# Performance work log

Measured on AMD Instinct MI355X. Metric: run time of the kernel, lower is better.

The kernel has to match this reference:

```python
import jax, jax.numpy as jnp
import numpy as np

NUM_HEADS = 16
HIDDEN = 1024
HEAD_DIM = HIDDEN // NUM_HEADS


def setup_inputs() -> dict:
    key = jax.random.key(0)
    ks = jax.random.split(key, 9)
    B, S, D = 2, 2048, HIDDEN
    scale = 1.0 / np.sqrt(D)
    inp = {
        "X": jax.random.normal(ks[0], (B, S, D), dtype=jnp.float32),
        "Wq": jax.random.normal(ks[1], (D, D), dtype=jnp.float32) * scale,
        "bq": jnp.zeros((D,), dtype=jnp.float32),
        "Wk": jax.random.normal(ks[2], (D, D), dtype=jnp.float32) * scale,
        "bk": jnp.zeros((D,), dtype=jnp.float32),
        "Wv": jax.random.normal(ks[3], (D, D), dtype=jnp.float32) * scale,
        "bv": jnp.zeros((D,), dtype=jnp.float32),
        "Wo": jax.random.normal(ks[4], (D, D), dtype=jnp.float32) * scale,
        "bo": jnp.zeros((D,), dtype=jnp.float32),
    }
    return inp


def _split_heads(x):
    b, s, d = x.shape
    return x.reshape(b, s, NUM_HEADS, HEAD_DIM).transpose(0, 2, 1, 3)  # [b,h,s,hd]


def reference(X, Wq, bq, Wk, bk, Wv, bv, Wo, bo):
    b, s, d = X.shape
    q = _split_heads(X @ Wq + bq)
    k = _split_heads(X @ Wk + bk)
    v = _split_heads(X @ Wv + bv)
    scores = jnp.einsum("bhqd,bhkd->bhqk", q, k) / jnp.sqrt(jnp.float32(HEAD_DIM))
    causal = jnp.tril(jnp.ones((s, s), dtype=bool))
    scores = jnp.where(causal[None, None], scores, jnp.float32(-jnp.inf))
    attn = jax.nn.softmax(scores, axis=-1)
    out = jnp.einsum("bhqk,bhkd->bhqd", attn, v)
    out = out.transpose(0, 2, 1, 3).reshape(b, s, d)
    return out @ Wo + bo
```

## Files before the change

kernel.cpp:

```cpp
#include <hip/hip_runtime.h>
#include <hip/hip_bf16.h>

#define S_LEN 2048
#define D_MODEL 1024
#define NHEAD 16
#define HDIM 64
#define BATCH 2
#define M_TOT (BATCH * S_LEN)
#define KVB 64

typedef __attribute__((ext_vector_type(4))) float f32x4;
typedef __attribute__((ext_vector_type(4))) short s16x4;
typedef __attribute__((ext_vector_type(8))) short s16x8;

#define AS1 __attribute__((address_space(1)))
#define AS3 __attribute__((address_space(3)))

#define SC2 0.18033688011112042f

__device__ inline short f2bf(float f) {
  unsigned u = __float_as_uint(f);
  return (short)((u + 0x7fffu + ((u >> 16) & 1u)) >> 16);
}

__device__ __forceinline__ unsigned cvtpk(float lo, float hi) {
  unsigned r;
  asm("v_cvt_pk_bf16_f32 %0, %1, %2" : "=v"(r) : "v"(lo), "v"(hi));
  return r;
}
__device__ __forceinline__ s16x4 pk4(float a, float b, float c, float d) {
  union { unsigned u[2]; s16x4 s; } x;
  x.u[0] = cvtpk(a, b);
  x.u[1] = cvtpk(c, d);
  return x.s;
}

__device__ __forceinline__ void gl_lds16(const short* g, short* l) {
  __builtin_amdgcn_global_load_lds((const AS1 void*)g, (AS3 void*)l, 16, 0, 0);
}

__global__ __launch_bounds__(256) void xcast_k(const float* __restrict__ X,
                                               short* __restrict__ Xb) {
  const size_t i = ((size_t)blockIdx.x * 256 + threadIdx.x) * 8;
  float4 a = *(const float4*)&X[i];
  float4 b = *(const float4*)&X[i + 4];
  s16x8 p;
  p[0] = f2bf(a.x); p[1] = f2bf(a.y); p[2] = f2bf(a.z); p[3] = f2bf(a.w);
  p[4] = f2bf(b.x); p[5] = f2bf(b.y); p[6] = f2bf(b.z); p[7] = f2bf(b.w);
  *(s16x8*)&Xb[i] = p;
}

__global__ __launch_bounds__(256) void wtrans_k(const float* __restrict__ W0,
                                                const float* __restrict__ W1,
                                                const float* __restrict__ W2,
                                                const float* __restrict__ W3,
                                                short* __restrict__ Wcat) {
  const int z = blockIdx.z;
  const float* W = z == 0 ? W0 : z == 1 ? W1 : z == 2 ? W2 : W3;
  short* Wt = Wcat + (size_t)z * D_MODEL * D_MODEL;
  const float scl = (z == 0) ? SC2 : 1.f;
  __shared__ float tile[32][33];
  const int tx = threadIdx.x, ty = threadIdx.y;
  const int n0 = blockIdx.x * 32, k0 = blockIdx.y * 32;
#pragma unroll
  for (int j = 0; j < 4; ++j)
    tile[ty + j * 8][tx] = W[(size_t)(k0 + ty + j * 8) * D_MODEL + n0 + tx];
  __syncthreads();
#pragma unroll
  for (int j = 0; j < 4; ++j)
    Wt[(size_t)(n0 + ty + j * 8) * D_MODEL + k0 + tx] =
        f2bf(tile[tx][ty + j * 8] * scl);
}

__global__ __launch_bounds__(256, 2) void gemm_qkv_k(
    const short* __restrict__ Xb, const short* __restrict__ Wcat,
    const float* __restrict__ bq, const float* __restrict__ bk,
    const float* __restrict__ bv, short* __restrict__ Qb,
    short* __restrict__ Kb, short* __restrict__ Vtb) {
  __shared__ short As[2 * 128 * 64];
  __shared__ short Bs[2 * 192 * 64];
  const int orig = blockIdx.x;
  const int xcd = orig & 7;
  const int k = orig >> 3;
  const int m0 = (((xcd & 3) << 3) + (k & 7)) * 128;
  const int n0 = (((xcd >> 2) << 3) + (k >> 3)) * 192;

  const int tid = threadIdx.x;
  const int lane = tid & 63, w = tid >> 6;
  const int wm = w >> 1, wn = w & 1;
  const int lr = lane & 15, lg = lane >> 4;
  const int lr8 = lane >> 3;
  const int sl = lane & 7;
  const int scol = ((sl ^ lr8) << 3);

  f32x4 acc[4][6] = {};

  auto stage = [&](int buf, int k0) {
#pragma unroll
    for (int j = 0; j < 4; ++j) {
      const int rb = j * 4 + w;
      const int row = rb * 8 + lr8;
      gl_lds16(&Xb[(size_t)(m0 + row) * D_MODEL + k0 + scol],
               &As[buf * 8192 + rb * 512]);
    }
#pragma unroll
    for (int j = 0; j < 6; ++j) {
      const int rb = j * 4 + w;
      const int row = rb * 8 + lr8;
      gl_lds16(&Wcat[(size_t)(n0 + row) * D_MODEL + k0 + scol],
               &Bs[buf * 12288 + rb * 512]);
    }
  };

  stage(0, 0);
  __syncthreads();

  for (int t = 0; t < D_MODEL / 64; ++t) {
    const int cur = t & 1;
    if (t + 1 < D_MODEL / 64) stage(cur ^ 1, (t + 1) * 64);
    const short* Ac = As + cur * 8192;
    const short* Bc = Bs + cur * 12288;
#pragma unroll
    for (int ks = 0; ks < 2; ++ks) {
      s16x8 af[4], bfr[6];
#pragma unroll
      for (int i = 0; i < 4; ++i) {
        const int Ra = wm * 64 + i * 16 + lr;
        af[i] = *(const s16x8*)&Ac[Ra * 64 + ((((ks << 2) | lg) ^ (Ra & 7)) << 3)];
      }
#pragma unroll
      for (int i = 0; i < 6; ++i) {
        const int Rb = wn * 96 + i * 16 + lr;
        bfr[i] = *(const s16x8*)&Bc[Rb * 64 + ((((ks << 2) | lg) ^ (Rb & 7)) << 3)];
      }
      __builtin_amdgcn_s_setprio(1);
#pragma unroll
      for (int mi = 0; mi < 4; ++mi)
#pragma unroll
        for (int ni = 0; ni < 6; ++ni)
          acc[mi][ni] = __builtin_amdgcn_mfma_f32_16x16x32_bf16(
              af[mi], bfr[ni], acc[mi][ni], 0, 0, 0);
      __builtin_amdgcn_s_setprio(0);
    }
    __syncthreads();
  }

#pragma unroll
  for (int ni = 0; ni < 6; ++ni) {
    const int n = n0 + wn * 96 + ni * 16 + lr;
    const int z = n >> 10;
    const float bn = (z == 0 ? bq[n & 1023] * SC2
                             : (z == 1 ? bk[n & 1023] : bv[n & 1023]));
    short* Cp = z == 0 ? Qb : z == 1 ? Kb : Vtb;
    const int h = (n >> 6) & 15, d = n & 63;
#pragma unroll
    for (int mi = 0; mi < 4; ++mi) {
      const int mb = m0 + wm * 64 + mi * 16 + lg * 4;
      f32x4 v = acc[mi][ni];
      if (z < 2) {
#pragma unroll
        for (int j = 0; j < 4; ++j) {
          int m = mb + j;
          int b = m >> 11, s = m & 2047;
          Cp[((size_t)((b * NHEAD + h) * S_LEN) + s) * HDIM + d] = f2bf(v[j] + bn);
        }
      } else {
        int b = mb >> 11, s = mb & 2047;
        s16x4 p;
#pragma unroll
        for (int j = 0; j < 4; ++j) p[j] = f2bf(v[j] + bn);
        *(s16x4*)&Cp[((size_t)((b * NHEAD + h) * HDIM) + d) * S_LEN + s] = p;
      }
    }
  }
}

__global__ __launch_bounds__(256, 2) void gemm_o_k(const short* __restrict__ A,
                                                   const short* __restrict__ Bt,
                                                   const float* __restrict__ bias,
                                                   float* __restrict__ C) {
  __shared__ short As[2 * 128 * 64];
  __shared__ short Bs[2 * 64 * 64];
  const int orig = blockIdx.x;
  const int xcd = orig & 7;
  const int k = orig >> 3;
  const int m0 = (((xcd & 3) << 3) + (k & 7)) * 128;
  const int n0 = (((xcd >> 2) << 3) + (k >> 3)) * 64;

  const int tid = threadIdx.x;
  const int lane = tid & 63, w = tid >> 6;
  const int wm = w >> 1, wn = w & 1;
  const int lr = lane & 15, lg = lane >> 4;
  const int lr8 = lane >> 3;
  const int sl = lane & 7;
  const int scol = ((sl ^ lr8) << 3);

  f32x4 acc[4][2] = {};

  auto stage = [&](int buf, int k0) {
#pragma unroll
    for (int j = 0; j < 4; ++j) {
      const int rb = j * 4 + w;
      const int row = rb * 8 + lr8;
      gl_lds16(&A[(size_t)(m0 + row) * D_MODEL + k0 + scol],
               &As[buf * 8192 + rb * 512]);
    }
#pragma unroll
    for (int j = 0; j < 2; ++j) {
      const int rb = j * 4 + w;
      const int row = rb * 8 + lr8;
      gl_lds16(&Bt[(size_t)(n0 + row) * D_MODEL + k0 + scol],
               &Bs[buf * 4096 + rb * 512]);
    }
  };

  stage(0, 0);
  __syncthreads();

  for (int t = 0; t < D_MODEL / 64; ++t) {
    const int cur = t & 1;
    if (t + 1 < D_MODEL / 64) stage(cur ^ 1, (t + 1) * 64);
    const short* Ac = As + cur * 8192;
    const short* Bc = Bs + cur * 4096;
#pragma unroll
    for (int ks = 0; ks < 2; ++ks) {
      s16x8 af[4], bfr[2];
#pragma unroll
      for (int i = 0; i < 4; ++i) {
        const int Ra = wm * 64 + i * 16 + lr;
        af[i] = *(const s16x8*)&Ac[Ra * 64 + ((((ks << 2) | lg) ^ (Ra & 7)) << 3)];
      }
#pragma unroll
      for (int i = 0; i < 2; ++i) {
        const int Rb = wn * 32 + i * 16 + lr;
        bfr[i] = *(const s16x8*)&Bc[Rb * 64 + ((((ks << 2) | lg) ^ (Rb & 7)) << 3)];
      }
      __builtin_amdgcn_s_setprio(1);
#pragma unroll
      for (int mi = 0; mi < 4; ++mi)
#pragma unroll
        for (int ni = 0; ni < 2; ++ni)
          acc[mi][ni] = __builtin_amdgcn_mfma_f32_16x16x32_bf16(
              af[mi], bfr[ni], acc[mi][ni], 0, 0, 0);
      __builtin_amdgcn_s_setprio(0);
    }
    __syncthreads();
  }

#pragma unroll
  for (int ni = 0; ni < 2; ++ni) {
    const int n = n0 + wn * 32 + ni * 16 + lr;
    const float bn = bias[n];
#pragma unroll
    for (int mi = 0; mi < 4; ++mi) {
      const int mb = m0 + wm * 64 + mi * 16 + lg * 4;
      f32x4 v = acc[mi][ni];
#pragma unroll
      for (int j = 0; j < 4; ++j)
        C[(size_t)(mb + j) * D_MODEL + n] = v[j] + bn;
    }
  }
}

__global__ __launch_bounds__(256, 4) void attn_k(const short* __restrict__ Q,
                                                 const short* __restrict__ K,
                                                 const short* __restrict__ Vt,
                                                 short* __restrict__ AO) {
  __shared__ short Ks[2][KVB * HDIM];
  __shared__ short Vs[2][HDIM * KVB];
  const int tid = threadIdx.x, w = tid >> 6, lane = tid & 63;
  const int lr = lane & 15, lg = lane >> 4;
  const int orig = blockIdx.x;
  const int wg = (orig & 7) * 128 + (orig >> 3);
  const int bh = wg >> 5, qi = wg & 31;
  const int qt = (bh & 1) ? qi : 31 - qi;
  const int q0 = qt * 64, nt = qt + 1;
  const int b = bh >> 4, h = bh & 15;
  const size_t headQK = (size_t)bh * S_LEN * HDIM;
  const size_t headV = (size_t)bh * HDIM * S_LEN;
  const int qrow = q0 + w * 16 + lr;

  const int l8 = lane >> 3, sl = lane & 7;
  const int scol = ((sl ^ l8) << 3);

  auto stage = [&](int kv0, int buf) {
#pragma unroll
    for (int j = 0; j < 2; ++j) {
      const int rb = w * 2 + j;
      const int row = rb * 8 + l8;
      gl_lds16(&K[headQK + (size_t)(kv0 + row) * HDIM + scol],
               &Ks[buf][rb * 512]);
      gl_lds16(&Vt[headV + (size_t)row * S_LEN + kv0 + scol],
               &Vs[buf][rb * 512]);
    }
  };

  const s16x8 qf0 = *(const s16x8*)&Q[headQK + (size_t)qrow * HDIM + lg * 8];
  const s16x8 qf1 = *(const s16x8*)&Q[headQK + (size_t)qrow * HDIM + 32 + lg * 8];

  f32x4 o[4] = {};
  float m_run = -1e30f;
  float l_part = 0.f;

  stage(0, 0);
  __syncthreads();

  for (int t = 0; t < nt; ++t) {
    if (t + 1 < nt) stage((t + 1) * KVB, (t + 1) & 1);
    const short* Kc = Ks[t & 1];
    const short* Vc = Vs[t & 1];
    const bool diag = (t == nt - 1);
    const int gmax = diag ? (w + 1) : 4;

    f32x4 sc[4];
    __builtin_amdgcn_s_setprio(1);
#pragma unroll
    for (int g = 0; g < 4; ++g) {
      if (g < gmax) {
        const int R = g * 16 + lr;
        const s16x8 kf0 = *(const s16x8*)&Kc[R * 64 + ((lg ^ (lr & 7)) << 3)];
        const s16x8 kf1 = *(const s16x8*)&Kc[R * 64 + (((4 | lg) ^ (lr & 7)) << 3)];
        f32x4 z = {0.f, 0.f, 0.f, 0.f};
        sc[g] = __builtin_amdgcn_mfma_f32_16x16x32_bf16(kf0, qf0, z, 0, 0, 0);
        sc[g] = __builtin_amdgcn_mfma_f32_16x16x32_bf16(kf1, qf1, sc[g], 0, 0, 0);
      }
    }
    __builtin_amdgcn_s_setprio(0);

    if (diag) {
#pragma unroll
      for (int g = 0; g < 4; ++g)
        if (g == w) {
#pragma unroll
          for (int j = 0; j < 4; ++j)
            if (lg * 4 + j > lr) sc[g][j] = -1e30f;
        }
    }

    float tm = -1e30f;
#pragma unroll
    for (int g = 0; g < 4; ++g)
      if (g < gmax)
        tm = fmaxf(tm, fmaxf(fmaxf(sc[g][0], sc[g][1]),
                             fmaxf(sc[g][2], sc[g][3])));

    if (!__all(tm <= m_run + 8.f)) {
      float tr = fmaxf(tm, m_run);
      tr = fmaxf(tr, __shfl_xor(tr, 16));
      tr = fmaxf(tr, __shfl_xor(tr, 32));
      const float corr = __builtin_amdgcn_exp2f(m_run - tr);
      l_part *= corr;
#pragma unroll
      for (int dc = 0; dc < 4; ++dc) o[dc] = o[dc] * corr;
      m_run = tr;
    }

    s16x4 pf[4];
#pragma unroll
    for (int g = 0; g < 4; ++g) {
      if (g < gmax) {
        const float e0 = __builtin_amdgcn_exp2f(sc[g][0] - m_run);
        const float e1 = __builtin_amdgcn_exp2f(sc[g][1] - m_run);
        const float e2 = __builtin_amdgcn_exp2f(sc[g][2] - m_run);
        const float e3 = __builtin_amdgcn_exp2f(sc[g][3] - m_run);
        pf[g] = pk4(e0, e1, e2, e3);
        l_part += (e0 + e1) + (e2 + e3);
      }
    }

    __builtin_amdgcn_s_setprio(1);
#pragma unroll
    for (int g = 0; g < 4; ++g) {
      if (g < gmax) {
#pragma unroll
        for (int dc = 0; dc < 4; ++dc) {
          const int row = dc * 16 + lr;
          const s16x4 vf = *(const s16x4*)&Vc[row * 64 +
              (((2 * g + (lg >> 1)) ^ (lr & 7)) << 3) + ((lg & 1) << 2)];
          o[dc] = __builtin_amdgcn_mfma_f32_16x16x16bf16_1k(vf, pf[g], o[dc], 0, 0, 0);
        }
      }
    }
    __builtin_amdgcn_s_setprio(0);
    __syncthreads();
  }

  float lt = l_part;
  lt += __shfl_xor(lt, 16);
  lt += __shfl_xor(lt, 32);
  const float inv = 1.f / lt;
#pragma unroll
  for (int dc = 0; dc < 4; ++dc) {
    s16x4 pk;
#pragma unroll
    for (int j = 0; j < 4; ++j) pk[j] = f2bf(o[dc][j] * inv);
    *(s16x4*)&AO[((size_t)(b * S_LEN + qrow)) * D_MODEL + h * HDIM + dc * 16 + lg * 4] = pk;
  }
}

extern "C" void kernel_launch(void* const* d_in, const int* in_sizes, int n_in,
                              void* d_out, int out_size, void* d_ws, size_t ws_size,
                              hipStream_t stream) {
  const float* X  = (const float*)d_in[0];
  const float* Wq = (const float*)d_in[1];
  const float* bq = (const float*)d_in[2];
  const float* Wk = (const float*)d_in[3];
  const float* bk = (const float*)d_in[4];
  const float* Wv = (const float*)d_in[5];
  const float* bv = (const float*)d_in[6];
  const float* Wo = (const float*)d_in[7];
  const float* bo = (const float*)d_in[8];
  (void)in_sizes; (void)n_in; (void)out_size; (void)ws_size;

  char* ws = (char*)d_ws;
  const size_t WSZ = (size_t)D_MODEL * D_MODEL * sizeof(short);
  const size_t QSZ = (size_t)M_TOT * D_MODEL * sizeof(short);
  short* Wcat = (short*)ws;
  short* Qb  = (short*)(ws + 4 * WSZ);
  short* Kb  = (short*)(ws + 4 * WSZ + QSZ);
  short* Vtb = (short*)(ws + 4 * WSZ + 2 * QSZ);
  short* AO  = (short*)(ws + 4 * WSZ + 3 * QSZ);
  short* Xb  = AO;
  short* Wto = Wcat + 3 * (size_t)D_MODEL * D_MODEL;

  xcast_k<<<dim3(M_TOT * D_MODEL / 2048), 256, 0, stream>>>(X, Xb);
  wtrans_k<<<dim3(32, 32, 4), dim3(32, 8), 0, stream>>>(Wq, Wk, Wv, Wo, Wcat);

  gemm_qkv_k<<<dim3(512), 256, 0, stream>>>(Xb, Wcat, bq, bk, bv,
                                            Qb, Kb, Vtb);

  attn_k<<<dim3(1024), 256, 0, stream>>>(Qb, Kb, Vtb, AO);

  gemm_o_k<<<dim3(512), 256, 0, stream>>>(AO, Wto, bo, (float*)d_out);
}
```

Baseline: 105.7 us.

## Prefetch two tiles ahead with explicit vmcnt waits in GEMMs and attention

The three kernels (QKV GEMM, output GEMM, attention) now issue loads for the next two tiles before entering the loop. Each iteration waits with s_waitcnt vmcnt(N) only for the older tile's direct-to-LDS loads, then uses raw s_barrier plus sched_barrier in place of __syncthreads. This gives a deeper in-flight load queue, so global-to-LDS copies overlap a full compute step instead of one. It depends on the hand-counted vmcnt values matching the exact number of loads each stage issues; a wrong count would create a race.

```diff
diff --git a/kernel.cpp b/kernel.cpp
--- a/kernel.cpp
+++ b/kernel.cpp
@@ -17,6 +17,8 @@
 #define AS3 __attribute__((address_space(3)))
 
 #define SC2 0.18033688011112042f
+
+#define WAITVM(N) asm volatile("s_waitcnt vmcnt(" #N ")" ::: "memory")
 
 __device__ inline short f2bf(float f) {
   unsigned u = __float_as_uint(f);
@@ -113,11 +115,13 @@
   };
 
   stage(0, 0);
-  __syncthreads();
+  stage(1, 64);
 
   for (int t = 0; t < D_MODEL / 64; ++t) {
     const int cur = t & 1;
-    if (t + 1 < D_MODEL / 64) stage(cur ^ 1, (t + 1) * 64);
+    if (t + 1 < D_MODEL / 64) { WAITVM(10); } else { WAITVM(0); }
+    __builtin_amdgcn_s_barrier();
+    __builtin_amdgcn_sched_barrier(0);
     const short* Ac = As + cur * 8192;
     const short* Bc = Bs + cur * 12288;
 #pragma unroll
@@ -142,7 +146,9 @@
               af[mi], bfr[ni], acc[mi][ni], 0, 0, 0);
       __builtin_amdgcn_s_setprio(0);
     }
-    __syncthreads();
+    __builtin_amdgcn_sched_barrier(0);
+    __builtin_amdgcn_s_barrier();
+    if (t + 2 < D_MODEL / 64) stage(cur, (t + 2) * 64);
   }
 
 #pragma unroll
@@ -215,11 +221,13 @@
   };
 
   stage(0, 0);
-  __syncthreads();
+  stage(1, 64);
 
   for (int t = 0; t < D_MODEL / 64; ++t) {
     const int cur = t & 1;
-    if (t + 1 < D_MODEL / 64) stage(cur ^ 1, (t + 1) * 64);
+    if (t + 1 < D_MODEL / 64) { WAITVM(6); } else { WAITVM(0); }
+    __builtin_amdgcn_s_barrier();
+    __builtin_amdgcn_sched_barrier(0);
     const short* Ac = As + cur * 8192;
     const short* Bc = Bs + cur * 4096;
 #pragma unroll
@@ -244,7 +252,9 @@
               af[mi], bfr[ni], acc[mi][ni], 0, 0, 0);
       __builtin_amdgcn_s_setprio(0);
     }
-    __syncthreads();
+    __builtin_amdgcn_sched_barrier(0);
+    __builtin_amdgcn_s_barrier();
+    if (t + 2 < D_MODEL / 64) stage(cur, (t + 2) * 64);
   }
 
 #pragma unroll
@@ -252,7 +262,7 @@
     const int n = n0 + wn * 32 + ni * 16 + lr;
     const float bn = bias[n];
 #pragma unroll
-    for (int mi = 0; mi < 4; ++mi) {
+    for (int mi = 0; mi < 2 * 2; ++mi) {
       const int mb = m0 + wm * 64 + mi * 16 + lg * 4;
       f32x4 v = acc[mi][ni];
 #pragma unroll
@@ -303,10 +313,12 @@
   float l_part = 0.f;
 
   stage(0, 0);
-  __syncthreads();
+  if (nt > 1) stage(KVB, 1);
 
   for (int t = 0; t < nt; ++t) {
-    if (t + 1 < nt) stage((t + 1) * KVB, (t + 1) & 1);
+    if (t + 1 < nt) { WAITVM(4); } else { WAITVM(0); }
+    __builtin_amdgcn_s_barrier();
+    __builtin_amdgcn_sched_barrier(0);
     const short* Kc = Ks[t & 1];
     const short* Vc = Vs[t & 1];
     const bool diag = (t == nt - 1);
@@ -382,7 +394,9 @@
       }
     }
     __builtin_amdgcn_s_setprio(0);
-    __syncthreads();
+    __builtin_amdgcn_sched_barrier(0);
+    __builtin_amdgcn_s_barrier();
+    if (t + 2 < nt) stage((t + 2) * KVB, t & 1);
   }
 
   float lt = l_part;
```

New measurement: 103.5 us. -2.1%, faster.

## Split KV range of long causal query tiles across two blocks with combine kernel

Applied to the files above, without the earlier changes.

Query tiles in the second half of the sequence now have their KV loop split into two halves, each run by a separate workgroup. The halves write unnormalized fp32 partial outputs plus running max and sum into scratch, and a new combine kernel merges them into bf16 attention output. The aim is to shorten the critical path of the longest causal tiles and balance work across CUs. The cost is an extra kernel launch, the fp32 partial traffic, and the loss of the previous heavy-first block ordering. Scratch is borrowed from the output buffer and from the already-consumed Wq region of the workspace.

```diff
diff --git a/kernel.cpp b/kernel.cpp
--- a/kernel.cpp
+++ b/kernel.cpp
@@ -265,16 +265,28 @@
 __global__ __launch_bounds__(256, 4) void attn_k(const short* __restrict__ Q,
                                                  const short* __restrict__ K,
                                                  const short* __restrict__ Vt,
-                                                 short* __restrict__ AO) {
+                                                 short* __restrict__ AO,
+                                                 float* __restrict__ opart,
+                                                 float* __restrict__ lmbuf) {
   __shared__ short Ks[2][KVB * HDIM];
   __shared__ short Vs[2][HDIM * KVB];
   const int tid = threadIdx.x, w = tid >> 6, lane = tid & 63;
   const int lr = lane & 15, lg = lane >> 4;
   const int orig = blockIdx.x;
-  const int wg = (orig & 7) * 128 + (orig >> 3);
-  const int bh = wg >> 5, qi = wg & 31;
-  const int qt = (bh & 1) ? qi : 31 - qi;
-  const int q0 = qt * 64, nt = qt + 1;
+  const int bh = orig & 31;
+  const int job = orig >> 5;
+  int qt, part, t0, te;
+  if (job < 16) {
+    qt = job; part = -1; t0 = 0; te = qt + 1;
+  } else {
+    qt = 16 + ((job - 16) >> 1);
+    part = (job - 16) & 1;
+    const int ntl = qt + 1, h0 = ntl >> 1;
+    t0 = part ? h0 : 0;
+    te = part ? ntl : h0;
+  }
+  const int nt = qt + 1;
+  const int q0 = qt * 64;
   const int b = bh >> 4, h = bh & 15;
   const size_t headQK = (size_t)bh * S_LEN * HDIM;
   const size_t headV = (size_t)bh * HDIM * S_LEN;
@@ -302,11 +314,11 @@
   float m_run = -1e30f;
   float l_part = 0.f;
 
-  stage(0, 0);
+  stage(t0 * KVB, t0 & 1);
   __syncthreads();
 
-  for (int t = 0; t < nt; ++t) {
-    if (t + 1 < nt) stage((t + 1) * KVB, (t + 1) & 1);
+  for (int t = t0; t < te; ++t) {
+    if (t + 1 < te) stage((t + 1) * KVB, (t + 1) & 1);
     const short* Kc = Ks[t & 1];
     const short* Vc = Vs[t & 1];
     const bool diag = (t == nt - 1);
@@ -388,13 +400,61 @@
   float lt = l_part;
   lt += __shfl_xor(lt, 16);
   lt += __shfl_xor(lt, 32);
-  const float inv = 1.f / lt;
-#pragma unroll
-  for (int dc = 0; dc < 4; ++dc) {
+
+  if (part < 0) {
+    const float inv = 1.f / lt;
+#pragma unroll
+    for (int dc = 0; dc < 4; ++dc) {
+      s16x4 pk;
+#pragma unroll
+      for (int j = 0; j < 4; ++j) pk[j] = f2bf(o[dc][j] * inv);
+      *(s16x4*)&AO[((size_t)(b * S_LEN + qrow)) * D_MODEL + h * HDIM + dc * 16 + lg * 4] = pk;
+    }
+  } else {
+    const int p = (bh * 16 + (qt - 16)) * 2 + part;
+    float* ob = opart + (size_t)p * 4096;
+    const int rloc = w * 16 + lr;
+#pragma unroll
+    for (int dc = 0; dc < 4; ++dc)
+      *(f32x4*)&ob[rloc * 64 + dc * 16 + lg * 4] = o[dc];
+    if (lane < 16) {
+      float* lm = lmbuf + (size_t)p * 128;
+      lm[rloc * 2 + 0] = m_run;
+      lm[rloc * 2 + 1] = lt;
+    }
+  }
+}
+
+__global__ __launch_bounds__(256) void attn_combine_k(
+    const float* __restrict__ opart, const float* __restrict__ lmbuf,
+    short* __restrict__ AO) {
+  const int blk = blockIdx.x;
+  const int bh = blk & 31, s = blk >> 5;
+  const int qt = 16 + s;
+  const int p0 = (bh * 16 + s) * 2;
+  const int tid = threadIdx.x;
+  const int r = tid >> 2, d0 = (tid & 3) * 16;
+  const float m0 = lmbuf[(size_t)p0 * 128 + r * 2];
+  const float l0 = lmbuf[(size_t)p0 * 128 + r * 2 + 1];
+  const float m1 = lmbuf[(size_t)(p0 + 1) * 128 + r * 2];
+  const float l1 = lmbuf[(size_t)(p0 + 1) * 128 + r * 2 + 1];
+  const float M = fmaxf(m0, m1);
+  const float w0 = __builtin_amdgcn_exp2f(m0 - M);
+  const float w1 = __builtin_amdgcn_exp2f(m1 - M);
+  const float inv = 1.f / (l0 * w0 + l1 * w1);
+  const float* o0 = opart + (size_t)p0 * 4096 + r * 64 + d0;
+  const float* o1 = opart + (size_t)(p0 + 1) * 4096 + r * 64 + d0;
+  const int b = bh >> 4, h = bh & 15;
+  const int qrow = qt * 64 + r;
+  short* dst = AO + ((size_t)(b * S_LEN + qrow)) * D_MODEL + h * HDIM + d0;
+#pragma unroll
+  for (int j = 0; j < 16; j += 4) {
+    f32x4 a = *(const f32x4*)&o0[j];
+    f32x4 c = *(const f32x4*)&o1[j];
     s16x4 pk;
 #pragma unroll
-    for (int j = 0; j < 4; ++j) pk[j] = f2bf(o[dc][j] * inv);
-    *(s16x4*)&AO[((size_t)(b * S_LEN + qrow)) * D_MODEL + h * HDIM + dc * 16 + lg * 4] = pk;
+    for (int q = 0; q < 4; ++q) pk[q] = f2bf((a[q] * w0 + c[q] * w1) * inv);
+    *(s16x4*)&dst[j] = pk;
   }
 }
 
@@ -423,13 +483,17 @@
   short* Xb  = AO;
   short* Wto = Wcat + 3 * (size_t)D_MODEL * D_MODEL;
 
+  float* opart = (float*)d_out;
+  float* lmbuf = (float*)ws;
+
   xcast_k<<<dim3(M_TOT * D_MODEL / 2048), 256, 0, stream>>>(X, Xb);
   wtrans_k<<<dim3(32, 32, 4), dim3(32, 8), 0, stream>>>(Wq, Wk, Wv, Wo, Wcat);
 
   gemm_qkv_k<<<dim3(512), 256, 0, stream>>>(Xb, Wcat, bq, bk, bv,
                                             Qb, Kb, Vtb);
 
-  attn_k<<<dim3(1024), 256, 0, stream>>>(Qb, Kb, Vtb, AO);
+  attn_k<<<dim3(1536), 256, 0, stream>>>(Qb, Kb, Vtb, AO, opart, lmbuf);
+  attn_combine_k<<<dim3(512), 256, 0, stream>>>(opart, lmbuf, AO);
 
   gemm_o_k<<<dim3(512), 256, 0, stream>>>(AO, Wto, bo, (float*)d_out);
 }
```

New measurement: 112.5 us. 6.4% more time.
